# Kernel tuning notes

Measured on AMD Instinct MI355X. Metric: run time of the kernel, lower is better.

Reference implementation:

```python
import jax, jax.numpy as jnp
import numpy as np

NUM_CLASSES = 16
ALPHA = 1.0
BETA = 1.0
GAMMA = 1.0
MARGIN = 1.0
B, D = 65536, 1024


def setup_inputs() -> dict:
    key = jax.random.key(0)
    k1, k2, k3 = jax.random.split(key, 3)
    logits = jax.random.normal(k1, (B, NUM_CLASSES), dtype=jnp.float32)
    features = jax.random.normal(k2, (B, D), dtype=jnp.float32)
    labels = jax.random.randint(k3, (B,), 0, NUM_CLASSES)
    return {"logits": logits, "labels": labels, "features": features}


def _total_loss(logits, features, labels):
    C = NUM_CLASSES
    dt = features.dtype
    # --- cross entropy (mean reduction, matches nn.CrossEntropyLoss) ---
    logp = jax.nn.log_softmax(logits, axis=-1)
    ce = -jnp.mean(jnp.take_along_axis(logp, labels[:, None], axis=1))
    # --- per-class counts / sums via single-pass segment reduce ---
    counts = jax.ops.segment_sum(jnp.ones((features.shape[0],), dt), labels, num_segments=C)  # [C]
    sums = jax.ops.segment_sum(features, labels, num_segments=C)  # [C, D]
    valid = counts > 0
    safe_counts = jnp.where(valid, counts, jnp.ones_like(counts))
    centroids = sums / safe_counts[:, None]  # [C, D]
    # --- intra-class: mean over valid classes of mean distance-to-centroid ---
    diffs = features - centroids[labels]  # [B, D]
    dists = jnp.sqrt(jnp.sum(diffs * diffs, axis=1))  # [B]
    per_class_mean_dist = jax.ops.segment_sum(dists, labels, num_segments=C) / safe_counts
    n_valid = jnp.sum(valid.astype(dt))
    intra = jnp.where(
        n_valid > 0,
        jnp.sum(jnp.where(valid, per_class_mean_dist, 0.0)) / jnp.maximum(n_valid, 1.0),
        jnp.zeros((), dt),
    )
    # --- inter-class: mean over valid (i<j) pairs of relu(margin - ||c_i - c_j||) ---
    pair_mask = (valid[:, None] & valid[None, :]) & (jnp.arange(C)[:, None] < jnp.arange(C)[None, :])
    d2 = jnp.sum((centroids[:, None, :] - centroids[None, :, :]) ** 2, axis=-1)  # [C, C]
    d2_safe = jnp.where(pair_mask, d2, jnp.ones_like(d2))  # avoid sqrt(0) on diagonal
    cdist = jnp.sqrt(d2_safe)
    inter_terms = jnp.where(pair_mask, jax.nn.relu(MARGIN - cdist), 0.0)
    n_pairs = jnp.sum(pair_mask.astype(dt))
    inter = jnp.where(
        n_pairs > 0,
        jnp.sum(inter_terms) / jnp.maximum(n_pairs, 1.0),
        jnp.zeros((), dt),
    )
    return ALPHA * ce + BETA * inter + GAMMA * intra


def reference(logits, labels, features):
    return _total_loss(logits, features, labels)
```

## Files before the change

### kernel.cpp

```cpp
#include <hip/hip_runtime.h>
#include <math.h>

#define NCLS      16
#define B_ROWS    65536
#define MARGINc   1.0f
#define CHUNK     64
#define CPC       128
#define NCHUNK    (NCLS * CPC)

#define F_CE     0
#define F_CNT    32
#define F_OFFS   48
#define F_INV    64
#define F_CEPART 256
#define F_HIST   1024
#define F_BASES  8192
#define F_CENT   16384
#define F_ORDER  32768
#define F_DISTP  98304
#define F_PART   131072

#define CADD(V) { acc.x += V.x; acc.y += V.y; acc.z += V.z; acc.w += V.w; }
#define DSQ(V, C) { float dx = V.x - C.x, dy = V.y - C.y, dz = V.z - C.z, dw = V.w - C.w; \
                    accT += dx * dx + dy * dy + dz * dz + dw * dw; }

__global__ __launch_bounds__(256) void k_ce_hist(const float* __restrict__ logits,
                                                 const int* __restrict__ labels,
                                                 float* __restrict__ ws) {
    __shared__ int hist[NCLS];
    __shared__ float cew[4];
    int tid = threadIdx.x, lane = tid & 63, w = tid >> 6;
    int b = blockIdx.x;
    if (tid < NCLS) hist[tid] = 0;
    __syncthreads();
    int row = b * 256 + tid;
    const float4* lg = (const float4*)(logits + (size_t)row * 16);
    float4 a = lg[0], b4 = lg[1], c = lg[2], d = lg[3];
    float m = fmaxf(fmaxf(fmaxf(a.x, a.y), fmaxf(a.z, a.w)),
                    fmaxf(fmaxf(b4.x, b4.y), fmaxf(b4.z, b4.w)));
    m = fmaxf(m, fmaxf(fmaxf(c.x, c.y), fmaxf(c.z, c.w)));
    m = fmaxf(m, fmaxf(fmaxf(d.x, d.y), fmaxf(d.z, d.w)));
    float s = expf(a.x - m) + expf(a.y - m) + expf(a.z - m) + expf(a.w - m)
            + expf(b4.x - m) + expf(b4.y - m) + expf(b4.z - m) + expf(b4.w - m)
            + expf(c.x - m) + expf(c.y - m) + expf(c.z - m) + expf(c.w - m)
            + expf(d.x - m) + expf(d.y - m) + expf(d.z - m) + expf(d.w - m);
    int lab = labels[row];
    atomicAdd(&hist[lab], 1);
    float xl = logits[(size_t)row * 16 + lab];
    float ce = (m + logf(s)) - xl;
    for (int o = 32; o >= 1; o >>= 1) ce += __shfl_down(ce, o, 64);
    if (lane == 0) cew[w] = ce;
    __syncthreads();
    if (tid == 0) ws[F_CEPART + b] = cew[0] + cew[1] + cew[2] + cew[3];
    if (tid < NCLS) ((int*)ws)[F_HIST + tid * 256 + b] = hist[tid];
}

__global__ __launch_bounds__(1024) void k_prefix(float* __restrict__ ws) {
    __shared__ int ctot[NCLS];
    __shared__ float cew[4];
    int tid = threadIdx.x, lane = tid & 63, w = tid >> 6;
    const int* hist = (const int*)ws + F_HIST;
    int* bases = (int*)ws + F_BASES;
    int base = lane * 4;
    int v0 = hist[w * 256 + base + 0];
    int v1 = hist[w * 256 + base + 1];
    int v2 = hist[w * 256 + base + 2];
    int v3 = hist[w * 256 + base + 3];
    int tot = v0 + v1 + v2 + v3;
    int x = tot;
    for (int o = 1; o < 64; o <<= 1) {
        int y = __shfl_up(x, o, 64);
        if (lane >= o) x += y;
    }
    int excl = x - tot;
    if (lane == 63) ctot[w] = x;
    __syncthreads();
    int off = 0;
    for (int cc = 0; cc < NCLS; ++cc) if (cc < w) off += ctot[cc];
    bases[w * 256 + base + 0] = off + excl;
    bases[w * 256 + base + 1] = off + excl + v0;
    bases[w * 256 + base + 2] = off + excl + v0 + v1;
    bases[w * 256 + base + 3] = off + excl + v0 + v1 + v2;
    if (lane == 0) {
        int cnt = ctot[w];
        ((int*)ws)[F_CNT + w] = cnt;
        ((int*)ws)[F_OFFS + w] = off;
        ws[F_INV + w] = 1.0f / (float)(cnt > 0 ? cnt : 1);
    }
    float s = (tid < 256) ? ws[F_CEPART + tid] : 0.f;
    if (tid < 256) {
        for (int o = 32; o >= 1; o >>= 1) s += __shfl_down(s, o, 64);
        if (lane == 0) cew[w] = s;
    }
    __syncthreads();
    if (tid == 0) ws[F_CE] = cew[0] + cew[1] + cew[2] + cew[3];
}

__global__ __launch_bounds__(256) void k_scatter(const int* __restrict__ labels,
                                                 float* __restrict__ ws) {
    __shared__ int cur[NCLS];
    int tid = threadIdx.x, b = blockIdx.x;
    if (tid < NCLS) cur[tid] = ((int*)ws)[F_BASES + tid * 256 + b];
    __syncthreads();
    int row = b * 256 + tid;
    int lab = labels[row];
    int pos = atomicAdd(&cur[lab], 1);
    ((int*)ws)[F_ORDER + pos] = row;
}

__global__ __launch_bounds__(256) void k_csums(const float* __restrict__ feat,
                                               float* __restrict__ ws) {
    int tid = threadIdx.x;
    int vc = blockIdx.x;
    int c = vc >> 7, k = vc & (CPC - 1);
    const int* cnts  = (const int*)ws + F_CNT;
    const int* offs  = (const int*)ws + F_OFFS;
    const int* order = (const int*)ws + F_ORDER;
    const float4* f4 = (const float4*)feat;
    float4* part4 = (float4*)(ws + F_PART);

    int cnt = cnts[c];
    int s0 = k * CHUNK;
    float4 acc = make_float4(0.f, 0.f, 0.f, 0.f);
    if (s0 < cnt) {
        int e = s0 + CHUNK; if (e > cnt) e = cnt;
        const int* ord = order + offs[c] + s0;
        int n = e - s0;
        int i = 0;
        for (; i + 8 <= n; i += 8) {
            int i0 = ord[i], i1 = ord[i + 1], i2 = ord[i + 2], i3 = ord[i + 3];
            int i4 = ord[i + 4], i5 = ord[i + 5], i6 = ord[i + 6], i7 = ord[i + 7];
            float4 v0 = f4[(size_t)i0 * 256 + tid];
            float4 v1 = f4[(size_t)i1 * 256 + tid];
            float4 v2 = f4[(size_t)i2 * 256 + tid];
            float4 v3 = f4[(size_t)i3 * 256 + tid];
            float4 v4 = f4[(size_t)i4 * 256 + tid];
            float4 v5 = f4[(size_t)i5 * 256 + tid];
            float4 v6 = f4[(size_t)i6 * 256 + tid];
            float4 v7 = f4[(size_t)i7 * 256 + tid];
            CADD(v0) CADD(v1) CADD(v2) CADD(v3)
            CADD(v4) CADD(v5) CADD(v6) CADD(v7)
        }
        for (; i < n; ++i) {
            float4 v = f4[(size_t)ord[i] * 256 + tid];
            CADD(v)
        }
    }
    part4[(size_t)vc * 256 + tid] = acc;
}

__global__ __launch_bounds__(256) void k_cent(float* __restrict__ ws) {
    int j = blockIdx.x * 256 + threadIdx.x;
    int c = j >> 10, d = j & 1023;
    int cnt = ((const int*)ws)[F_CNT + c];
    int kmax = (cnt + CHUNK - 1) >> 6;
    const float* part = ws + F_PART + (size_t)c * CPC * 1024 + d;
    float s = 0.f;
    int k = 0;
    for (; k + 4 <= kmax; k += 4)
        s += part[(size_t)k * 1024] + part[(size_t)(k + 1) * 1024]
           + part[(size_t)(k + 2) * 1024] + part[(size_t)(k + 3) * 1024];
    for (; k < kmax; ++k) s += part[(size_t)k * 1024];
    ws[F_CENT + j] = s * ws[F_INV + c];
}

__global__ __launch_bounds__(256) void k_dist(const float* __restrict__ feat,
                                              float* __restrict__ ws) {
    __shared__ float red[4];
    int tid = threadIdx.x, lane = tid & 63, w = tid >> 6;
    int vc = (NCHUNK - 1) - blockIdx.x;
    int c = vc >> 7, k = vc & (CPC - 1);
    const int* cnts  = (const int*)ws + F_CNT;
    const int* offs  = (const int*)ws + F_OFFS;
    const int* order = (const int*)ws + F_ORDER;
    const float4* f4 = (const float4*)feat;
    const float4* c4 = (const float4*)(ws + F_CENT);
    float* distp = ws + F_DISTP;

    int cnt = cnts[c];
    int s0 = k * CHUNK;
    if (s0 >= cnt) { if (tid == 0) distp[vc] = 0.f; return; }
    int n = cnt - s0; if (n > CHUNK) n = CHUNK;
    const int* ord = order + offs[c] + s0;

    float4 c0 = c4[c * 256 + 0 * 64 + lane];
    float4 c1 = c4[c * 256 + 1 * 64 + lane];
    float4 c2 = c4[c * 256 + 2 * 64 + lane];
    float4 c3 = c4[c * 256 + 3 * 64 + lane];

    float wsum = 0.f;
    int rbeg = w * 16;
    int rend = rbeg + 16; if (rend > n) rend = n;
    int i = rbeg;
    for (; i + 2 <= rend; i += 2) {
        int ra = ord[i], rb = ord[i + 1];
        float4 va0 = f4[(size_t)ra * 256 + 0 * 64 + lane];
        float4 va1 = f4[(size_t)ra * 256 + 1 * 64 + lane];
        float4 va2 = f4[(size_t)ra * 256 + 2 * 64 + lane];
        float4 va3 = f4[(size_t)ra * 256 + 3 * 64 + lane];
        float4 vb0 = f4[(size_t)rb * 256 + 0 * 64 + lane];
        float4 vb1 = f4[(size_t)rb * 256 + 1 * 64 + lane];
        float4 vb2 = f4[(size_t)rb * 256 + 2 * 64 + lane];
        float4 vb3 = f4[(size_t)rb * 256 + 3 * 64 + lane];
        float accT;
        accT = 0.f; DSQ(va0, c0) DSQ(va1, c1) DSQ(va2, c2) DSQ(va3, c3)
        float accA = accT;
        accT = 0.f; DSQ(vb0, c0) DSQ(vb1, c1) DSQ(vb2, c2) DSQ(vb3, c3)
        float accB = accT;
        for (int o = 32; o >= 1; o >>= 1) {
            accA += __shfl_down(accA, o, 64);
            accB += __shfl_down(accB, o, 64);
        }
        if (lane == 0) wsum += sqrtf(accA) + sqrtf(accB);
    }
    if (i < rend) {
        int ra = ord[i];
        float4 va0 = f4[(size_t)ra * 256 + 0 * 64 + lane];
        float4 va1 = f4[(size_t)ra * 256 + 1 * 64 + lane];
        float4 va2 = f4[(size_t)ra * 256 + 2 * 64 + lane];
        float4 va3 = f4[(size_t)ra * 256 + 3 * 64 + lane];
        float accT = 0.f;
        DSQ(va0, c0) DSQ(va1, c1) DSQ(va2, c2) DSQ(va3, c3)
        for (int o = 32; o >= 1; o >>= 1) accT += __shfl_down(accT, o, 64);
        if (lane == 0) wsum += sqrtf(accT);
    }
    if (lane == 0) red[w] = wsum;
    __syncthreads();
    if (tid == 0) distp[vc] = red[0] + red[1] + red[2] + red[3];
}

__global__ __launch_bounds__(256) void k_final(float* __restrict__ ws, float* __restrict__ out) {
    __shared__ float red[256];
    __shared__ float winter[4];
    __shared__ int wcnt[4];
    int tid = threadIdx.x, lane = tid & 63, w = tid >> 6;
    const int* cnts = (const int*)ws + F_CNT;

    int c0 = tid & 15, g = tid >> 4;
    const float* dp = ws + F_DISTP;
    float s = 0.f;
    for (int k = g; k < CPC; k += 16) s += dp[(c0 << 7) + k];
    red[tid] = s;
    __syncthreads();

    const float4* c4 = (const float4*)(ws + F_CENT);
    float interAcc = 0.f; int pairAcc = 0;
    for (int p = w; p < 120; p += 4) {
        int i = 0, rem = p;
        while (rem >= 15 - i) { rem -= 15 - i; ++i; }
        int j = i + 1 + rem;
        int ci = cnts[i], cj = cnts[j];
        float acc = 0.f;
#pragma unroll
        for (int k = 0; k < 4; ++k) {
            float4 a = c4[i * 256 + k * 64 + lane];
            float4 b = c4[j * 256 + k * 64 + lane];
            float dx = a.x - b.x, dy = a.y - b.y, dz = a.z - b.z, dw = a.w - b.w;
            acc += dx * dx + dy * dy + dz * dz + dw * dw;
        }
        for (int o = 32; o >= 1; o >>= 1) acc += __shfl_down(acc, o, 64);
        if (lane == 0 && ci > 0 && cj > 0) {
            float t = MARGINc - sqrtf(acc);
            if (t > 0.f) interAcc += t;
            pairAcc += 1;
        }
    }
    if (lane == 0) { winter[w] = interAcc; wcnt[w] = pairAcc; }
    __syncthreads();
    if (tid == 0) {
        float interSum = winter[0] + winter[1] + winter[2] + winter[3];
        int np = wcnt[0] + wcnt[1] + wcnt[2] + wcnt[3];
        float inter = np > 0 ? interSum / (float)np : 0.f;
        float intra = 0.f; int nv = 0;
        for (int cc = 0; cc < NCLS; ++cc) {
            float dsum = 0.f;
            for (int gg = 0; gg < 16; ++gg) dsum += red[gg * 16 + cc];
            if (cnts[cc] > 0) { intra += dsum * ws[F_INV + cc]; nv++; }
        }
        intra = nv > 0 ? intra / (float)nv : 0.f;
        float ce = ws[F_CE] / (float)B_ROWS;
        out[0] = ce + inter + intra;
    }
}

extern "C" void kernel_launch(void* const* d_in, const int* in_sizes, int n_in,
                              void* d_out, int out_size, void* d_ws, size_t ws_size,
                              hipStream_t stream) {
    const float* logits = (const float*)d_in[0];
    const int* labels   = (const int*)d_in[1];
    const float* feat   = (const float*)d_in[2];
    float* ws  = (float*)d_ws;
    float* out = (float*)d_out;

    hipLaunchKernelGGL(k_ce_hist, dim3(256),    dim3(256),  0, stream, logits, labels, ws);
    hipLaunchKernelGGL(k_prefix,  dim3(1),      dim3(1024), 0, stream, ws);
    hipLaunchKernelGGL(k_scatter, dim3(256),    dim3(256),  0, stream, labels, ws);
    hipLaunchKernelGGL(k_csums,   dim3(NCHUNK), dim3(256),  0, stream, feat, ws);
    hipLaunchKernelGGL(k_cent,    dim3(64),     dim3(256),  0, stream, ws);
    hipLaunchKernelGGL(k_dist,    dim3(NCHUNK), dim3(256),  0, stream, feat, ws);
    hipLaunchKernelGGL(k_final,   dim3(1),      dim3(256),  0, stream, ws, out);
}
```

Measured before the change: 138.5 us.

## Fold prefix and final kernels into last-block epilogues via atomic counters

Removes the separate single-block prefix-scan and final-reduction kernels. Their work now runs in the last block to finish k_ce_hist and k_dist, which is detected with a threadfence and an atomic counter reset by a memset. Scatter now adds the per-class offset itself, and k_cent is relaunched with 128 blocks of 128 threads. This saves two kernel launches and their serialization gaps, at the cost of an extra memset, fences and atomics in every block.

New measurement: 425.8 us. 208% more time.

```diff
diff --git a/kernel.cpp b/kernel.cpp
--- a/kernel.cpp
+++ b/kernel.cpp
@@ -12,6 +12,8 @@
 #define F_CNT    32
 #define F_OFFS   48
 #define F_INV    64
+#define F_CTR    128
+#define F_CTR2   129
 #define F_CEPART 256
 #define F_HIST   1024
 #define F_BASES  8192
@@ -29,8 +31,11 @@
                                                  float* __restrict__ ws) {
     __shared__ int hist[NCLS];
     __shared__ float cew[4];
+    __shared__ int ctot[NCLS];
+    __shared__ int islast;
     int tid = threadIdx.x, lane = tid & 63, w = tid >> 6;
     int b = blockIdx.x;
+    int* wsi = (int*)ws;
     if (tid < NCLS) hist[tid] = 0;
     __syncthreads();
     int row = b * 256 + tid;
@@ -52,46 +57,49 @@
     if (lane == 0) cew[w] = ce;
     __syncthreads();
     if (tid == 0) ws[F_CEPART + b] = cew[0] + cew[1] + cew[2] + cew[3];
-    if (tid < NCLS) ((int*)ws)[F_HIST + tid * 256 + b] = hist[tid];
-}
-
-__global__ __launch_bounds__(1024) void k_prefix(float* __restrict__ ws) {
-    __shared__ int ctot[NCLS];
-    __shared__ float cew[4];
-    int tid = threadIdx.x, lane = tid & 63, w = tid >> 6;
-    const int* hist = (const int*)ws + F_HIST;
-    int* bases = (int*)ws + F_BASES;
-    int base = lane * 4;
-    int v0 = hist[w * 256 + base + 0];
-    int v1 = hist[w * 256 + base + 1];
-    int v2 = hist[w * 256 + base + 2];
-    int v3 = hist[w * 256 + base + 3];
-    int tot = v0 + v1 + v2 + v3;
-    int x = tot;
-    for (int o = 1; o < 64; o <<= 1) {
-        int y = __shfl_up(x, o, 64);
-        if (lane >= o) x += y;
-    }
-    int excl = x - tot;
-    if (lane == 63) ctot[w] = x;
-    __syncthreads();
-    int off = 0;
-    for (int cc = 0; cc < NCLS; ++cc) if (cc < w) off += ctot[cc];
-    bases[w * 256 + base + 0] = off + excl;
-    bases[w * 256 + base + 1] = off + excl + v0;
-    bases[w * 256 + base + 2] = off + excl + v0 + v1;
-    bases[w * 256 + base + 3] = off + excl + v0 + v1 + v2;
-    if (lane == 0) {
-        int cnt = ctot[w];
-        ((int*)ws)[F_CNT + w] = cnt;
-        ((int*)ws)[F_OFFS + w] = off;
-        ws[F_INV + w] = 1.0f / (float)(cnt > 0 ? cnt : 1);
-    }
-    float s = (tid < 256) ? ws[F_CEPART + tid] : 0.f;
-    if (tid < 256) {
-        for (int o = 32; o >= 1; o >>= 1) s += __shfl_down(s, o, 64);
-        if (lane == 0) cew[w] = s;
-    }
+    if (tid < NCLS) wsi[F_HIST + tid * 256 + b] = hist[tid];
+
+    __threadfence();
+    if (tid == 0) islast = (atomicAdd(wsi + F_CTR, 1) == 255);
+    __syncthreads();
+    if (!islast) return;
+    __threadfence();
+    const int* histg = wsi + F_HIST;
+    int* bases = wsi + F_BASES;
+    for (int ci = 0; ci < 4; ++ci) {
+        int cc = w * 4 + ci;
+        int base = lane * 4;
+        int v0 = histg[cc * 256 + base + 0];
+        int v1 = histg[cc * 256 + base + 1];
+        int v2 = histg[cc * 256 + base + 2];
+        int v3 = histg[cc * 256 + base + 3];
+        int tot = v0 + v1 + v2 + v3;
+        int x = tot;
+        for (int o = 1; o < 64; o <<= 1) {
+            int y = __shfl_up(x, o, 64);
+            if (lane >= o) x += y;
+        }
+        int excl = x - tot;
+        bases[cc * 256 + base + 0] = excl;
+        bases[cc * 256 + base + 1] = excl + v0;
+        bases[cc * 256 + base + 2] = excl + v0 + v1;
+        bases[cc * 256 + base + 3] = excl + v0 + v1 + v2;
+        if (lane == 63) ctot[cc] = x;
+    }
+    __syncthreads();
+    if (tid == 0) {
+        int off = 0;
+        for (int cc = 0; cc < NCLS; ++cc) {
+            int cnt = ctot[cc];
+            wsi[F_CNT + cc] = cnt;
+            wsi[F_OFFS + cc] = off;
+            ws[F_INV + cc] = 1.0f / (float)(cnt > 0 ? cnt : 1);
+            off += cnt;
+        }
+    }
+    float sv = ws[F_CEPART + tid];
+    for (int o = 32; o >= 1; o >>= 1) sv += __shfl_down(sv, o, 64);
+    if (lane == 0) cew[w] = sv;
     __syncthreads();
     if (tid == 0) ws[F_CE] = cew[0] + cew[1] + cew[2] + cew[3];
 }
@@ -100,12 +108,13 @@
                                                  float* __restrict__ ws) {
     __shared__ int cur[NCLS];
     int tid = threadIdx.x, b = blockIdx.x;
-    if (tid < NCLS) cur[tid] = ((int*)ws)[F_BASES + tid * 256 + b];
+    int* wsi = (int*)ws;
+    if (tid < NCLS) cur[tid] = wsi[F_OFFS + tid] + wsi[F_BASES + tid * 256 + b];
     __syncthreads();
     int row = b * 256 + tid;
     int lab = labels[row];
     int pos = atomicAdd(&cur[lab], 1);
-    ((int*)ws)[F_ORDER + pos] = row;
+    wsi[F_ORDER + pos] = row;
 }
 
 __global__ __launch_bounds__(256) void k_csums(const float* __restrict__ feat,
@@ -149,8 +158,8 @@
     part4[(size_t)vc * 256 + tid] = acc;
 }
 
-__global__ __launch_bounds__(256) void k_cent(float* __restrict__ ws) {
-    int j = blockIdx.x * 256 + threadIdx.x;
+__global__ __launch_bounds__(128) void k_cent(float* __restrict__ ws) {
+    int j = blockIdx.x * 128 + threadIdx.x;
     int c = j >> 10, d = j & 1023;
     int cnt = ((const int*)ws)[F_CNT + c];
     int kmax = (cnt + CHUNK - 1) >> 6;
@@ -165,85 +174,88 @@
 }
 
 __global__ __launch_bounds__(256) void k_dist(const float* __restrict__ feat,
-                                              float* __restrict__ ws) {
-    __shared__ float red[4];
+                                              float* __restrict__ ws,
+                                              float* __restrict__ out) {
+    __shared__ float red4[4];
+    __shared__ float redf[256];
+    __shared__ float winter[4];
+    __shared__ int wcnt[4];
+    __shared__ int islast;
     int tid = threadIdx.x, lane = tid & 63, w = tid >> 6;
     int vc = (NCHUNK - 1) - blockIdx.x;
     int c = vc >> 7, k = vc & (CPC - 1);
-    const int* cnts  = (const int*)ws + F_CNT;
-    const int* offs  = (const int*)ws + F_OFFS;
-    const int* order = (const int*)ws + F_ORDER;
+    int* wsi = (int*)ws;
+    const int* cnts  = wsi + F_CNT;
+    const int* offs  = wsi + F_OFFS;
+    const int* order = wsi + F_ORDER;
     const float4* f4 = (const float4*)feat;
     const float4* c4 = (const float4*)(ws + F_CENT);
     float* distp = ws + F_DISTP;
 
     int cnt = cnts[c];
     int s0 = k * CHUNK;
-    if (s0 >= cnt) { if (tid == 0) distp[vc] = 0.f; return; }
-    int n = cnt - s0; if (n > CHUNK) n = CHUNK;
-    const int* ord = order + offs[c] + s0;
-
-    float4 c0 = c4[c * 256 + 0 * 64 + lane];
-    float4 c1 = c4[c * 256 + 1 * 64 + lane];
-    float4 c2 = c4[c * 256 + 2 * 64 + lane];
-    float4 c3 = c4[c * 256 + 3 * 64 + lane];
-
-    float wsum = 0.f;
-    int rbeg = w * 16;
-    int rend = rbeg + 16; if (rend > n) rend = n;
-    int i = rbeg;
-    for (; i + 2 <= rend; i += 2) {
-        int ra = ord[i], rb = ord[i + 1];
-        float4 va0 = f4[(size_t)ra * 256 + 0 * 64 + lane];
-        float4 va1 = f4[(size_t)ra * 256 + 1 * 64 + lane];
-        float4 va2 = f4[(size_t)ra * 256 + 2 * 64 + lane];
-        float4 va3 = f4[(size_t)ra * 256 + 3 * 64 + lane];
-        float4 vb0 = f4[(size_t)rb * 256 + 0 * 64 + lane];
-        float4 vb1 = f4[(size_t)rb * 256 + 1 * 64 + lane];
-        float4 vb2 = f4[(size_t)rb * 256 + 2 * 64 + lane];
-        float4 vb3 = f4[(size_t)rb * 256 + 3 * 64 + lane];
-        float accT;
-        accT = 0.f; DSQ(va0, c0) DSQ(va1, c1) DSQ(va2, c2) DSQ(va3, c3)
-        float accA = accT;
-        accT = 0.f; DSQ(vb0, c0) DSQ(vb1, c1) DSQ(vb2, c2) DSQ(vb3, c3)
-        float accB = accT;
-        for (int o = 32; o >= 1; o >>= 1) {
-            accA += __shfl_down(accA, o, 64);
-            accB += __shfl_down(accB, o, 64);
-        }
-        if (lane == 0) wsum += sqrtf(accA) + sqrtf(accB);
-    }
-    if (i < rend) {
-        int ra = ord[i];
-        float4 va0 = f4[(size_t)ra * 256 + 0 * 64 + lane];
-        float4 va1 = f4[(size_t)ra * 256 + 1 * 64 + lane];
-        float4 va2 = f4[(size_t)ra * 256 + 2 * 64 + lane];
-        float4 va3 = f4[(size_t)ra * 256 + 3 * 64 + lane];
-        float accT = 0.f;
-        DSQ(va0, c0) DSQ(va1, c1) DSQ(va2, c2) DSQ(va3, c3)
-        for (int o = 32; o >= 1; o >>= 1) accT += __shfl_down(accT, o, 64);
-        if (lane == 0) wsum += sqrtf(accT);
-    }
-    if (lane == 0) red[w] = wsum;
-    __syncthreads();
-    if (tid == 0) distp[vc] = red[0] + red[1] + red[2] + red[3];
-}
-
-__global__ __launch_bounds__(256) void k_final(float* __restrict__ ws, float* __restrict__ out) {
-    __shared__ float red[256];
-    __shared__ float winter[4];
-    __shared__ int wcnt[4];
-    int tid = threadIdx.x, lane = tid & 63, w = tid >> 6;
-    const int* cnts = (const int*)ws + F_CNT;
+    if (s0 >= cnt) {
+        if (tid == 0) distp[vc] = 0.f;
+    } else {
+        int n = cnt - s0; if (n > CHUNK) n = CHUNK;
+        const int* ord = order + offs[c] + s0;
+        float4 c0 = c4[c * 256 + 0 * 64 + lane];
+        float4 c1 = c4[c * 256 + 1 * 64 + lane];
+        float4 c2 = c4[c * 256 + 2 * 64 + lane];
+        float4 c3 = c4[c * 256 + 3 * 64 + lane];
+        float wsum = 0.f;
+        int rbeg = w * 16;
+        int rend = rbeg + 16; if (rend > n) rend = n;
+        int i = rbeg;
+        for (; i + 2 <= rend; i += 2) {
+            int ra = ord[i], rb = ord[i + 1];
+            float4 va0 = f4[(size_t)ra * 256 + 0 * 64 + lane];
+            float4 va1 = f4[(size_t)ra * 256 + 1 * 64 + lane];
+            float4 va2 = f4[(size_t)ra * 256 + 2 * 64 + lane];
+            float4 va3 = f4[(size_t)ra * 256 + 3 * 64 + lane];
+            float4 vb0 = f4[(size_t)rb * 256 + 0 * 64 + lane];
+            float4 vb1 = f4[(size_t)rb * 256 + 1 * 64 + lane];
+            float4 vb2 = f4[(size_t)rb * 256 + 2 * 64 + lane];
+            float4 vb3 = f4[(size_t)rb * 256 + 3 * 64 + lane];
+            float accT;
+            accT = 0.f; DSQ(va0, c0) DSQ(va1, c1) DSQ(va2, c2) DSQ(va3, c3)
+            float accA = accT;
+            accT = 0.f; DSQ(vb0, c0) DSQ(vb1, c1) DSQ(vb2, c2) DSQ(vb3, c3)
+            float accB = accT;
+            for (int o = 32; o >= 1; o >>= 1) {
+                accA += __shfl_down(accA, o, 64);
+                accB += __shfl_down(accB, o, 64);
+            }
+            if (lane == 0) wsum += sqrtf(accA) + sqrtf(accB);
+        }
+        if (i < rend) {
+            int ra = ord[i];
+            float4 va0 = f4[(size_t)ra * 256 + 0 * 64 + lane];
+            float4 va1 = f4[(size_t)ra * 256 + 1 * 64 + lane];
+            float4 va2 = f4[(size_t)ra * 256 + 2 * 64 + lane];
+            float4 va3 = f4[(size_t)ra * 256 + 3 * 64 + lane];
+            float accT = 0.f;
+            DSQ(va0, c0) DSQ(va1, c1) DSQ(va2, c2) DSQ(va3, c3)
+            for (int o = 32; o >= 1; o >>= 1) accT += __shfl_down(accT, o, 64);
+            if (lane == 0) wsum += sqrtf(accT);
+        }
+        if (lane == 0) red4[w] = wsum;
+        __syncthreads();
+        if (tid == 0) distp[vc] = red4[0] + red4[1] + red4[2] + red4[3];
+    }
+
+    __threadfence();
+    if (tid == 0) islast = (atomicAdd(wsi + F_CTR2, 1) == NCHUNK - 1);
+    __syncthreads();
+    if (!islast) return;
+    __threadfence();
 
     int c0 = tid & 15, g = tid >> 4;
-    const float* dp = ws + F_DISTP;
     float s = 0.f;
-    for (int k = g; k < CPC; k += 16) s += dp[(c0 << 7) + k];
-    red[tid] = s;
-    __syncthreads();
-
-    const float4* c4 = (const float4*)(ws + F_CENT);
+    for (int kk = g; kk < CPC; kk += 16) s += distp[(c0 << 7) + kk];
+    redf[tid] = s;
+    __syncthreads();
+
     float interAcc = 0.f; int pairAcc = 0;
     for (int p = w; p < 120; p += 4) {
         int i = 0, rem = p;
@@ -252,9 +264,9 @@
         int ci = cnts[i], cj = cnts[j];
         float acc = 0.f;
 #pragma unroll
-        for (int k = 0; k < 4; ++k) {
-            float4 a = c4[i * 256 + k * 64 + lane];
-            float4 b = c4[j * 256 + k * 64 + lane];
+        for (int kk = 0; kk < 4; ++kk) {
+            float4 a = c4[i * 256 + kk * 64 + lane];
+            float4 b = c4[j * 256 + kk * 64 + lane];
             float dx = a.x - b.x, dy = a.y - b.y, dz = a.z - b.z, dw = a.w - b.w;
             acc += dx * dx + dy * dy + dz * dz + dw * dw;
         }
@@ -274,7 +286,7 @@
         float intra = 0.f; int nv = 0;
         for (int cc = 0; cc < NCLS; ++cc) {
             float dsum = 0.f;
-            for (int gg = 0; gg < 16; ++gg) dsum += red[gg * 16 + cc];
+            for (int gg = 0; gg < 16; ++gg) dsum += redf[gg * 16 + cc];
             if (cnts[cc] > 0) { intra += dsum * ws[F_INV + cc]; nv++; }
         }
         intra = nv > 0 ? intra / (float)nv : 0.f;
@@ -292,11 +304,11 @@
     float* ws  = (float*)d_ws;
     float* out = (float*)d_out;
 
-    hipLaunchKernelGGL(k_ce_hist, dim3(256),    dim3(256),  0, stream, logits, labels, ws);
-    hipLaunchKernelGGL(k_prefix,  dim3(1),      dim3(1024), 0, stream, ws);
-    hipLaunchKernelGGL(k_scatter, dim3(256),    dim3(256),  0, stream, labels, ws);
-    hipLaunchKernelGGL(k_csums,   dim3(NCHUNK), dim3(256),  0, stream, feat, ws);
-    hipLaunchKernelGGL(k_cent,    dim3(64),     dim3(256),  0, stream, ws);
-    hipLaunchKernelGGL(k_dist,    dim3(NCHUNK), dim3(256),  0, stream, feat, ws);
-    hipLaunchKernelGGL(k_final,   dim3(1),      dim3(256),  0, stream, ws, out);
-}
+    hipMemsetAsync((char*)d_ws + F_CTR * 4, 0, 8, stream);
+
+    hipLaunchKernelGGL(k_ce_hist, dim3(256),    dim3(256), 0, stream, logits, labels, ws);
+    hipLaunchKernelGGL(k_scatter, dim3(256),    dim3(256), 0, stream, labels, ws);
+    hipLaunchKernelGGL(k_csums,   dim3(NCHUNK), dim3(256), 0, stream, feat, ws);
+    hipLaunchKernelGGL(k_cent,    dim3(128),    dim3(128), 0, stream, ws);
+    hipLaunchKernelGGL(k_dist,    dim3(NCHUNK), dim3(256), 0, stream, feat, ws, out);
+}
```
